# Kernel tuning notes

Measured on AMD Instinct MI355X. Metric: run time of the kernel, lower is better.

The kernel has to match this reference:

```python
import jax, jax.numpy as jnp
import numpy as np

N_X = 32640   # total xlmr subword tokens (64 seqs x 510 tokens)
N_S = 16320   # total stanza word tokens (2 subwords per word)
E = 65280     # dependency edges (bidirectional, avg degree ~4)
D = 768
GCN_DIM = 256
GCN_NUM = 2
POS_DIM = 4
N_UPOS = 17
N_LABEL = 5


def setup_inputs() -> dict:
    key = jax.random.key(0)
    ks = jax.random.split(key, 8)
    x = jax.random.normal(ks[0], (N_X, D), dtype=jnp.float32)
    # mapStanza2Xlmr as segment ids: xlmr token j belongs to stanza word j//2
    seg = jnp.arange(N_X, dtype=jnp.int32) // 2
    edge_index = jax.random.randint(ks[1], (2, E), 0, N_S, dtype=jnp.int32)
    upos_ids = jax.random.randint(ks[2], (N_S,), 0, N_UPOS, dtype=jnp.int32)
    Wc = jax.random.normal(ks[3], (D, GCN_DIM), dtype=jnp.float32) * 0.02
    bc = jnp.zeros((GCN_DIM,), dtype=jnp.float32)
    gcn_W = jax.random.normal(ks[4], (GCN_NUM, GCN_DIM, GCN_DIM), dtype=jnp.float32) * 0.05
    gcn_b = jnp.zeros((GCN_NUM, GCN_DIM), dtype=jnp.float32)
    upos_table = jax.random.normal(ks[5], (N_UPOS, POS_DIM), dtype=jnp.float32)
    Wcls = jax.random.normal(ks[6], (D + GCN_DIM + POS_DIM, N_LABEL), dtype=jnp.float32) * 0.02
    bcls = jnp.zeros((N_LABEL,), dtype=jnp.float32)
    return {"x": x, "seg": seg, "edge_index": edge_index, "upos_ids": upos_ids,
            "Wc": Wc, "bc": bc, "gcn_W": gcn_W, "gcn_b": gcn_b,
            "upos_table": upos_table, "Wcls": Wcls, "bcls": bcls}


def _gcn_conv(h, srcs, dsts, W, b, n):
    # PyG GCNConv: h' = D^-1/2 (A+I) D^-1/2 (h W) + b  (self loops already in srcs/dsts)
    h = h @ W
    deg = jax.ops.segment_sum(jnp.ones_like(dsts, h.dtype), dsts, num_segments=n)
    dinv = jax.lax.rsqrt(deg)  # deg >= 1 because of self loops
    coef = dinv[srcs] * dinv[dsts]
    out = jax.ops.segment_sum(h[srcs] * coef[:, None], dsts, num_segments=n)
    return out + b


def reference(x, seg, edge_index, upos_ids, Wc, bc, gcn_W, gcn_b, upos_table, Wcls, bcls):
    # mapStanza2Xlmr: mean-pool subword embeddings into stanza word embeddings
    cnt = jax.ops.segment_sum(jnp.ones((N_X,), x.dtype), seg, num_segments=N_S)
    stanza = jax.ops.segment_sum(x, seg, num_segments=N_S) / cnt[:, None]  # [N_S, D]
    # GCN over dependency edges (gcn_mode=0: biedges)
    h = stanza @ Wc + bc
    self_idx = jnp.arange(N_S, dtype=edge_index.dtype)
    srcs = jnp.concatenate([edge_index[0], self_idx])
    dsts = jnp.concatenate([edge_index[1], self_idx])
    for i in range(GCN_NUM):
        h = jax.nn.relu(_gcn_conv(h, srcs, dsts, gcn_W[i], gcn_b[i], N_S))
    # POS embedding + concat + relu
    pos = upos_table[upos_ids]                                  # [N_S, POS_DIM]
    info = jax.nn.relu(jnp.concatenate([h, pos], axis=1))       # [N_S, GCN_DIM+POS_DIM]
    # mapXlmr2Stanza: each subword gathers its (single) word's info
    append = info[seg]                                          # [N_X, GCN_DIM+POS_DIM]
    tok = jnp.concatenate([x, append], axis=1)                  # [N_X, 1028]
    logits = jax.nn.relu(tok) @ Wcls + bcls
    return jax.nn.log_softmax(logits, axis=1)
```

## Files before the change

### kernel.cpp

```cpp
#include <hip/hip_runtime.h>

#define NXT 32640
#define NS  16320
#define NE  65280
#define DD  768
#define GD  256
#define NLAB 5
#define CAP 32

typedef __attribute__((ext_vector_type(8))) short bf16x8;
typedef __attribute__((ext_vector_type(4))) float f32x4;

__device__ inline unsigned short f2b(float f) {
    unsigned int u = __float_as_uint(f);
    unsigned int r = (u + 0x7FFFu + ((u >> 16) & 1u)) >> 16;
    return (unsigned short)r;
}
__device__ inline float b2f(unsigned short h) {
    return __uint_as_float((unsigned int)h << 16);
}

__device__ inline void tile_transpose(const float* __restrict__ src, unsigned short* __restrict__ dst,
                                      int K, int k0, int n0, int tid) {
    __shared__ unsigned short tl[64][65];
#pragma unroll
    for (int i = 0; i < 16; ++i) {
        int idx = tid + i * 256;
        int r = idx >> 6, c = idx & 63;
        tl[r][c] = f2b(src[(size_t)(k0 + r) * GD + n0 + c]);
    }
    __syncthreads();
#pragma unroll
    for (int i = 0; i < 16; ++i) {
        int idx = tid + i * 256;
        int rr = idx >> 6, cc = idx & 63;
        dst[(size_t)(n0 + rr) * K + k0 + cc] = tl[cc][rr];
    }
}

__global__ void k_setup(int* __restrict__ cnt,
                        const float* __restrict__ Wc, unsigned short* __restrict__ WcT,
                        const float* __restrict__ gcn_W, unsigned short* __restrict__ WT,
                        const float* __restrict__ Wcls, float* __restrict__ WclsT,
                        const float* __restrict__ upos_table, const float* __restrict__ bcls,
                        float* __restrict__ posLogit) {
    int b = blockIdx.x, t = threadIdx.x;
    if (b < 64) {
        int i = b * 256 + t;
        if (i < NS) cnt[i] = 0;
    } else if (b < 112) {
        int tile = b - 64;
        tile_transpose(Wc, WcT, DD, (tile >> 2) * 64, (tile & 3) * 64, t);
    } else if (b < 128) {
        int tile = b - 112;
        tile_transpose(gcn_W, WT, GD, (tile >> 2) * 64, (tile & 3) * 64, t);
    } else if (b < 144) {
        int tile = b - 128;
        tile_transpose(gcn_W + (size_t)GD * GD, WT + (size_t)GD * GD, GD,
                       (tile >> 2) * 64, (tile & 3) * 64, t);
    } else if (b < 159) {
        int idx = (b - 144) * 256 + t;
        int l = idx / DD, k = idx - l * DD;
        WclsT[idx] = Wcls[(size_t)k * NLAB + l];
    } else {
        if (t < 17 * NLAB) {
            int u = t / NLAB, l = t - u * NLAB;
            float a = bcls[l];
#pragma unroll
            for (int p = 0; p < 4; ++p) {
                float pv = upos_table[u * 4 + p];
                pv = pv > 0.f ? pv : 0.f;
                a += pv * Wcls[(size_t)(DD + GD + p) * NLAB + l];
            }
            posLogit[t] = a;
        }
    }
}

__global__ void k_fill(const int* __restrict__ ei, int* __restrict__ cnt,
                       int* __restrict__ csr_src) {
    int e = blockIdx.x * 256 + threadIdx.x;
    if (e < NE) {
        int dst = ei[NE + e];
        int slot = atomicAdd(&cnt[dst], 1);
        if (slot < CAP) csr_src[(size_t)dst * CAP + slot] = ei[e];
    }
}

__global__ __launch_bounds__(256) void k_xpass(const float* __restrict__ x,
                                               const float* __restrict__ WclsT,
                                               float* __restrict__ partial,
                                               unsigned short* __restrict__ stanza) {
    int w    = blockIdx.x * 4 + (threadIdx.x >> 6);
    int lane = threadIdx.x & 63;
    const float* xr0 = x + (size_t)(2 * w) * DD + lane * 4;
    const float* xr1 = xr0 + DD;
    f32x4 a[3], b[3];
#pragma unroll
    for (int p = 0; p < 3; ++p) {
        a[p] = *(const f32x4*)(xr0 + p * 256);
        b[p] = *(const f32x4*)(xr1 + p * 256);
    }
#pragma unroll
    for (int p = 0; p < 3; ++p) {
        ushort4 o;
        o.x = f2b((a[p][0] + b[p][0]) * 0.5f);
        o.y = f2b((a[p][1] + b[p][1]) * 0.5f);
        o.z = f2b((a[p][2] + b[p][2]) * 0.5f);
        o.w = f2b((a[p][3] + b[p][3]) * 0.5f);
        *(ushort4*)(stanza + (size_t)w * DD + p * 256 + lane * 4) = o;
    }
    f32x4 ra[3], rb[3];
#pragma unroll
    for (int p = 0; p < 3; ++p)
#pragma unroll
        for (int i = 0; i < 4; ++i) {
            ra[p][i] = a[p][i] > 0.f ? a[p][i] : 0.f;
            rb[p][i] = b[p][i] > 0.f ? b[p][i] : 0.f;
        }
    float acc0[NLAB] = {}, acc1[NLAB] = {};
#pragma unroll
    for (int l = 0; l < NLAB; ++l)
#pragma unroll
        for (int p = 0; p < 3; ++p) {
            f32x4 wv = *(const f32x4*)(WclsT + (size_t)l * DD + p * 256 + lane * 4);
#pragma unroll
            for (int i = 0; i < 4; ++i) {
                acc0[l] += ra[p][i] * wv[i];
                acc1[l] += rb[p][i] * wv[i];
            }
        }
#pragma unroll
    for (int off = 32; off > 0; off >>= 1)
#pragma unroll
        for (int l = 0; l < NLAB; ++l) {
            acc0[l] += __shfl_xor(acc0[l], off);
            acc1[l] += __shfl_xor(acc1[l], off);
        }
    if (lane == 0) {
        float* pp = partial + (size_t)w * 2 * NLAB;
#pragma unroll
        for (int l = 0; l < NLAB; ++l) { pp[l] = acc0[l]; pp[NLAB + l] = acc1[l]; }
    }
}

__global__ __launch_bounds__(256) void k_gemm(const unsigned short* __restrict__ A,
                                              const unsigned short* __restrict__ BT,
                                              const float* __restrict__ bias,
                                              unsigned short* __restrict__ out,
                                              int K, int nbn) {
    __shared__ unsigned short lds[1536 * 8];
    const int tid  = threadIdx.x;
    const int lane = tid & 63;
    const int wv   = tid >> 6;
    const int wr   = wv >> 1, wc = wv & 1;
    const int bm   = (blockIdx.x / nbn) * 64;
    const int bn   = (blockIdx.x % nbn) * 128;

    const int g  = tid >> 6, w_ = tid & 63, kc = w_ >> 4, rl = w_ & 15;
    const unsigned short* srcA  = A  + (size_t)(bm + g * 16 + rl) * K + kc * 8;
    const unsigned short* srcB0 = BT + (size_t)(bn      + g * 16 + rl) * K + kc * 8;
    const unsigned short* srcB1 = BT + (size_t)(bn + 64 + g * 16 + rl) * K + kc * 8;

    unsigned short* dA0 = lds + (size_t)tid * 8;
    unsigned short* dA1 = dA0 + 256 * 8;
    unsigned short* dB  = lds + (size_t)(512 + tid) * 8;

    const bf16x8* fA = (const bf16x8*)lds + (wr * 2) * 64 + lane;
    const bf16x8* fB = (const bf16x8*)lds + 512 + wc * 256 + lane;

    f32x4 acc[2][4] = {};
    for (int k0 = 0; k0 < K; k0 += 64) {
        __builtin_amdgcn_global_load_lds(srcA  + k0,      dA0,            16, 0, 0);
        __builtin_amdgcn_global_load_lds(srcA  + k0 + 32, dA1,            16, 0, 0);
        __builtin_amdgcn_global_load_lds(srcB0 + k0,      dB,             16, 0, 0);
        __builtin_amdgcn_global_load_lds(srcB1 + k0,      dB + 256 * 8,   16, 0, 0);
        __builtin_amdgcn_global_load_lds(srcB0 + k0 + 32, dB + 512 * 8,   16, 0, 0);
        __builtin_amdgcn_global_load_lds(srcB1 + k0 + 32, dB + 768 * 8,   16, 0, 0);
        __syncthreads();
#pragma unroll
        for (int kh = 0; kh < 2; ++kh) {
            bf16x8 a0 = fA[kh * 256], a1 = fA[kh * 256 + 64];
            const bf16x8* fb = fB + kh * 512;
            bf16x8 b0 = fb[0], b1 = fb[64], b2 = fb[128], b3 = fb[192];
            acc[0][0] = __builtin_amdgcn_mfma_f32_16x16x32_bf16(a0, b0, acc[0][0], 0, 0, 0);
            acc[0][1] = __builtin_amdgcn_mfma_f32_16x16x32_bf16(a0, b1, acc[0][1], 0, 0, 0);
            acc[0][2] = __builtin_amdgcn_mfma_f32_16x16x32_bf16(a0, b2, acc[0][2], 0, 0, 0);
            acc[0][3] = __builtin_amdgcn_mfma_f32_16x16x32_bf16(a0, b3, acc[0][3], 0, 0, 0);
            acc[1][0] = __builtin_amdgcn_mfma_f32_16x16x32_bf16(a1, b0, acc[1][0], 0, 0, 0);
            acc[1][1] = __builtin_amdgcn_mfma_f32_16x16x32_bf16(a1, b1, acc[1][1], 0, 0, 0);
            acc[1][2] = __builtin_amdgcn_mfma_f32_16x16x32_bf16(a1, b2, acc[1][2], 0, 0, 0);
            acc[1][3] = __builtin_amdgcn_mfma_f32_16x16x32_bf16(a1, b3, acc[1][3], 0, 0, 0);
        }
        __syncthreads();
    }

    const int rl2 = lane & 15, rq = lane >> 4;
#pragma unroll
    for (int m = 0; m < 2; ++m) {
        int row0 = bm + wr * 32 + m * 16 + rq * 4;
#pragma unroll
        for (int n = 0; n < 4; ++n) {
            int col = bn + wc * 64 + n * 16 + rl2;
            float bv = bias ? bias[col] : 0.f;
#pragma unroll
            for (int r = 0; r < 4; ++r)
                out[(size_t)(row0 + r) * GD + col] = f2b(acc[m][n][r] + bv);
        }
    }
}

__global__ void k_gather(const int* __restrict__ cnt, const int* __restrict__ csr_src,
                         const unsigned short* __restrict__ hW,
                         const float* __restrict__ b, unsigned short* __restrict__ hout) {
    int w    = blockIdx.x * 4 + (threadIdx.x >> 6);
    int lane = threadIdx.x & 63;
    int c = cnt[w];
    float dw = rsqrtf((float)c + 1.0f);
    const int* sl = csr_src + (size_t)w * CAP;
    float ax = 0.f, ay = 0.f, az = 0.f, aw = 0.f;
    for (int j = 0; j < c; ++j) {
        int src = sl[j];
        float cf = rsqrtf((float)cnt[src] + 1.0f) * dw;
        ushort4 v = *(const ushort4*)&hW[(size_t)src * GD + lane * 4];
        ax += cf * b2f(v.x); ay += cf * b2f(v.y); az += cf * b2f(v.z); aw += cf * b2f(v.w);
    }
    ushort4 sv = *(const ushort4*)&hW[(size_t)w * GD + lane * 4];
    f32x4 bv = *(const f32x4*)&b[lane * 4];
    float c2 = dw * dw;
    float rx = ax + b2f(sv.x) * c2 + bv[0];
    float ry = ay + b2f(sv.y) * c2 + bv[1];
    float rz = az + b2f(sv.z) * c2 + bv[2];
    float rw = aw + b2f(sv.w) * c2 + bv[3];
    ushort4 o;
    o.x = f2b(rx > 0.f ? rx : 0.f);
    o.y = f2b(ry > 0.f ? ry : 0.f);
    o.z = f2b(rz > 0.f ? rz : 0.f);
    o.w = f2b(rw > 0.f ? rw : 0.f);
    *(ushort4*)&hout[(size_t)w * GD + lane * 4] = o;
}

__global__ void k_gather_final(const int* __restrict__ cnt, const int* __restrict__ csr_src,
                               const unsigned short* __restrict__ hW,
                               const float* __restrict__ b,
                               const float* __restrict__ partial,
                               const int* __restrict__ upos_ids,
                               const float* __restrict__ posLogit,
                               const float* __restrict__ Wcls,
                               float* __restrict__ out) {
    int w    = blockIdx.x * 4 + (threadIdx.x >> 6);
    int lane = threadIdx.x & 63;
    int c = cnt[w];
    float dw = rsqrtf((float)c + 1.0f);
    const int* sl = csr_src + (size_t)w * CAP;
    float ax = 0.f, ay = 0.f, az = 0.f, aw = 0.f;
    for (int j = 0; j < c; ++j) {
        int src = sl[j];
        float cf = rsqrtf((float)cnt[src] + 1.0f) * dw;
        ushort4 v = *(const ushort4*)&hW[(size_t)src * GD + lane * 4];
        ax += cf * b2f(v.x); ay += cf * b2f(v.y); az += cf * b2f(v.z); aw += cf * b2f(v.w);
    }
    ushort4 sv = *(const ushort4*)&hW[(size_t)w * GD + lane * 4];
    f32x4 bv = *(const f32x4*)&b[lane * 4];
    float c2 = dw * dw;
    float hv[4];
    hv[0] = ax + b2f(sv.x) * c2 + bv[0];
    hv[1] = ay + b2f(sv.y) * c2 + bv[1];
    hv[2] = az + b2f(sv.z) * c2 + bv[2];
    hv[3] = aw + b2f(sv.w) * c2 + bv[3];
    float acc[NLAB] = {};
#pragma unroll
    for (int i = 0; i < 4; ++i) {
        float v = hv[i] > 0.f ? hv[i] : 0.f;
        const float* wr = Wcls + (size_t)(DD + lane * 4 + i) * NLAB;
#pragma unroll
        for (int l = 0; l < NLAB; ++l) acc[l] += v * wr[l];
    }
#pragma unroll
    for (int off = 32; off > 0; off >>= 1)
#pragma unroll
        for (int l = 0; l < NLAB; ++l) acc[l] += __shfl_xor(acc[l], off);
    if (lane == 0) {
        const float* pl = posLogit + (size_t)upos_ids[w] * NLAB;
        const float* pp = partial + (size_t)w * 2 * NLAB;
#pragma unroll
        for (int t = 0; t < 2; ++t) {
            float lg[NLAB];
#pragma unroll
            for (int l = 0; l < NLAB; ++l) lg[l] = acc[l] + pp[t * NLAB + l] + pl[l];
            float m = lg[0];
#pragma unroll
            for (int l = 1; l < NLAB; ++l) m = fmaxf(m, lg[l]);
            float s = 0.f;
#pragma unroll
            for (int l = 0; l < NLAB; ++l) s += __expf(lg[l] - m);
            float lse = __logf(s) + m;
            float* op = out + (size_t)(2 * w + t) * NLAB;
#pragma unroll
            for (int l = 0; l < NLAB; ++l) op[l] = lg[l] - lse;
        }
    }
}

extern "C" void kernel_launch(void* const* d_in, const int* in_sizes, int n_in,
                              void* d_out, int out_size, void* d_ws, size_t ws_size,
                              hipStream_t stream) {
    const float* x          = (const float*)d_in[0];
    const int*   ei         = (const int*)d_in[2];
    const int*   upos_ids   = (const int*)d_in[3];
    const float* Wc         = (const float*)d_in[4];
    const float* bc         = (const float*)d_in[5];
    const float* gcn_W      = (const float*)d_in[6];
    const float* gcn_b      = (const float*)d_in[7];
    const float* upos_table = (const float*)d_in[8];
    const float* Wcls       = (const float*)d_in[9];
    const float* bcls       = (const float*)d_in[10];
    float* out = (float*)d_out;

    char* ws = (char*)d_ws;
    float* partial          = (float*)ws;            ws += (size_t)NXT * NLAB * 4;
    float* WclsT            = (float*)ws;            ws += (size_t)NLAB * DD * 4;
    float* posLogit         = (float*)ws;            ws += (size_t)17 * NLAB * 4;
    unsigned short* stanza  = (unsigned short*)ws;   ws += (size_t)NS * DD * 2;
    unsigned short* h_bf    = (unsigned short*)ws;   ws += (size_t)NS * GD * 2;
    unsigned short* hW_bf   = (unsigned short*)ws;   ws += (size_t)NS * GD * 2;
    unsigned short* WcT     = (unsigned short*)ws;   ws += (size_t)DD * GD * 2;
    unsigned short* WT      = (unsigned short*)ws;   ws += (size_t)2 * GD * GD * 2;
    int* cnt                = (int*)ws;              ws += (size_t)NS * 4;
    int* csr_src            = (int*)ws;              ws += (size_t)NS * CAP * 4;

    k_setup<<<160, 256, 0, stream>>>(cnt, Wc, WcT, gcn_W, WT, Wcls, WclsT,
                                     upos_table, bcls, posLogit);
    k_fill<<<(NE + 255) / 256, 256, 0, stream>>>(ei, cnt, csr_src);
    k_xpass<<<NS / 4, 256, 0, stream>>>(x, WclsT, partial, stanza);
    k_gemm<<<(NS / 64) * 2, 256, 0, stream>>>(stanza, WcT, bc, h_bf, DD, 2);
    k_gemm<<<(NS / 64) * 2, 256, 0, stream>>>(h_bf, WT, nullptr, hW_bf, GD, 2);
    k_gather<<<NS / 4, 256, 0, stream>>>(cnt, csr_src, hW_bf, gcn_b, h_bf);
    k_gemm<<<(NS / 64) * 2, 256, 0, stream>>>(h_bf, WT + (size_t)GD * GD, nullptr, hW_bf, GD, 2);
    k_gather_final<<<NS / 4, 256, 0, stream>>>(cnt, csr_src, hW_bf, gcn_b + GD,
                                               partial, upos_ids, posLogit, Wcls, out);
}
```

Baseline: 117.1 us.

## Fuse mean-pooling, Wc GEMM, classifier partial logits and CSR fill into one kernel

Merges the x-pass (mean pooling plus per-token classifier dot products), the first dense GEMM and the edge CSR fill into a single launch. Pooled bf16 rows go straight into LDS as the A operand, so the bf16 stanza intermediate is never written to or read back from global memory. The per-token classifier logits now run on MFMA against a zero-padded bf16 Wcls layout built in setup. The cost is more LDS per block, a bf16 rounding of the relu'd x before the classifier dot product, and a single 64-row tile computing all 256 output columns per block.

```diff
diff --git a/kernel.cpp b/kernel.cpp
--- a/kernel.cpp
+++ b/kernel.cpp
@@ -9,6 +9,7 @@
 #define CAP 32
 
 typedef __attribute__((ext_vector_type(8))) short bf16x8;
+typedef __attribute__((ext_vector_type(8))) unsigned short u16x8;
 typedef __attribute__((ext_vector_type(4))) float f32x4;
 
 __device__ inline unsigned short f2b(float f) {
@@ -41,7 +42,7 @@
 __global__ void k_setup(int* __restrict__ cnt,
                         const float* __restrict__ Wc, unsigned short* __restrict__ WcT,
                         const float* __restrict__ gcn_W, unsigned short* __restrict__ WT,
-                        const float* __restrict__ Wcls, float* __restrict__ WclsT,
+                        const float* __restrict__ Wcls, unsigned short* __restrict__ WclsF,
                         const float* __restrict__ upos_table, const float* __restrict__ bcls,
                         float* __restrict__ posLogit) {
     int b = blockIdx.x, t = threadIdx.x;
@@ -58,10 +59,12 @@
         int tile = b - 128;
         tile_transpose(gcn_W + (size_t)GD * GD, WT + (size_t)GD * GD, GD,
                        (tile >> 2) * 64, (tile & 3) * 64, t);
-    } else if (b < 159) {
+    } else if (b < 192) {
         int idx = (b - 144) * 256 + t;
-        int l = idx / DD, k = idx - l * DD;
-        WclsT[idx] = Wcls[(size_t)k * NLAB + l];
+        int i = idx & 7, l = (idx >> 3) & 63, s = idx >> 9;
+        int col = l & 15;
+        int k = s * 32 + (l >> 4) * 8 + i;
+        WclsF[idx] = (col < NLAB) ? f2b(Wcls[(size_t)k * NLAB + col]) : 0;
     } else {
         if (t < 17 * NLAB) {
             int u = t / NLAB, l = t - u * NLAB;
@@ -77,70 +80,113 @@
     }
 }
 
-__global__ void k_fill(const int* __restrict__ ei, int* __restrict__ cnt,
-                       int* __restrict__ csr_src) {
-    int e = blockIdx.x * 256 + threadIdx.x;
-    if (e < NE) {
-        int dst = ei[NE + e];
-        int slot = atomicAdd(&cnt[dst], 1);
-        if (slot < CAP) csr_src[(size_t)dst * CAP + slot] = ei[e];
-    }
-}
-
-__global__ __launch_bounds__(256) void k_xpass(const float* __restrict__ x,
-                                               const float* __restrict__ WclsT,
-                                               float* __restrict__ partial,
-                                               unsigned short* __restrict__ stanza) {
-    int w    = blockIdx.x * 4 + (threadIdx.x >> 6);
-    int lane = threadIdx.x & 63;
-    const float* xr0 = x + (size_t)(2 * w) * DD + lane * 4;
+__global__ __launch_bounds__(256) void k_mega0(const float* __restrict__ x,
+                                               const unsigned short* __restrict__ WcT,
+                                               const unsigned short* __restrict__ WclsF,
+                                               const float* __restrict__ bc,
+                                               const int* __restrict__ ei,
+                                               int* __restrict__ cnt, int* __restrict__ csr_src,
+                                               unsigned short* __restrict__ h_bf,
+                                               float* __restrict__ partial) {
+    __shared__ unsigned short lds[3584 * 8];
+    const int tid = threadIdx.x;
+    if (blockIdx.x >= 255) {
+        int e = (blockIdx.x - 255) * 256 + tid;
+        if (e < NE) {
+            int dst = ei[NE + e];
+            int slot = atomicAdd(&cnt[dst], 1);
+            if (slot < CAP) csr_src[(size_t)dst * CAP + slot] = ei[e];
+        }
+        return;
+    }
+    const int lane = tid & 63;
+    const int wv   = tid >> 6;
+    const int wr   = wv >> 1, wc = wv & 1;
+    const int bm   = blockIdx.x * 64;
+
+    const int g = tid >> 6, kc = (tid >> 4) & 3, rl = tid & 15;
+    const int w_loc = g * 16 + rl;
+    const float* xr0 = x + (size_t)(2 * (bm + w_loc)) * DD + kc * 8;
     const float* xr1 = xr0 + DD;
-    f32x4 a[3], b[3];
-#pragma unroll
-    for (int p = 0; p < 3; ++p) {
-        a[p] = *(const f32x4*)(xr0 + p * 256);
-        b[p] = *(const f32x4*)(xr1 + p * 256);
-    }
-#pragma unroll
-    for (int p = 0; p < 3; ++p) {
-        ushort4 o;
-        o.x = f2b((a[p][0] + b[p][0]) * 0.5f);
-        o.y = f2b((a[p][1] + b[p][1]) * 0.5f);
-        o.z = f2b((a[p][2] + b[p][2]) * 0.5f);
-        o.w = f2b((a[p][3] + b[p][3]) * 0.5f);
-        *(ushort4*)(stanza + (size_t)w * DD + p * 256 + lane * 4) = o;
-    }
-    f32x4 ra[3], rb[3];
-#pragma unroll
-    for (int p = 0; p < 3; ++p)
-#pragma unroll
-        for (int i = 0; i < 4; ++i) {
-            ra[p][i] = a[p][i] > 0.f ? a[p][i] : 0.f;
-            rb[p][i] = b[p][i] > 0.f ? b[p][i] : 0.f;
-        }
-    float acc0[NLAB] = {}, acc1[NLAB] = {};
-#pragma unroll
-    for (int l = 0; l < NLAB; ++l)
-#pragma unroll
-        for (int p = 0; p < 3; ++p) {
-            f32x4 wv = *(const f32x4*)(WclsT + (size_t)l * DD + p * 256 + lane * 4);
+    const int t0 = 2 * w_loc, t1 = t0 + 1;
+    const int ap0 = (t0 >> 4) * 64 + kc * 16 + (t0 & 15);
+    const int ap1 = (t1 >> 4) * 64 + kc * 16 + (t1 & 15);
+    const unsigned short* srcB = WcT + (size_t)(g * 16 + rl) * DD + kc * 8;
+
+    const bf16x8* ldsv = (const bf16x8*)lds;
+    f32x4 acc[2][8] = {};
+    f32x4 acc_lg[2] = {};
+
+    for (int it = 0; it < 12; ++it) {
+        const int k0 = it * 64;
+#pragma unroll
+        for (int nh = 0; nh < 4; ++nh)
+#pragma unroll
+            for (int kh = 0; kh < 2; ++kh)
+                __builtin_amdgcn_global_load_lds(srcB + (size_t)nh * 64 * DD + k0 + kh * 32,
+                                                 lds + (size_t)(1536 + (nh * 2 + kh) * 256 + tid) * 8,
+                                                 16, 0, 0);
+#pragma unroll
+        for (int kh = 0; kh < 2; ++kh) {
+            f32x4 v0a = *(const f32x4*)(xr0 + k0 + kh * 32);
+            f32x4 v0b = *(const f32x4*)(xr0 + k0 + kh * 32 + 4);
+            f32x4 v1a = *(const f32x4*)(xr1 + k0 + kh * 32);
+            f32x4 v1b = *(const f32x4*)(xr1 + k0 + kh * 32 + 4);
+            u16x8 pool, ra, rb;
 #pragma unroll
             for (int i = 0; i < 4; ++i) {
-                acc0[l] += ra[p][i] * wv[i];
-                acc1[l] += rb[p][i] * wv[i];
+                pool[i]     = f2b((v0a[i] + v1a[i]) * 0.5f);
+                pool[4 + i] = f2b((v0b[i] + v1b[i]) * 0.5f);
+                ra[i]     = f2b(v0a[i] > 0.f ? v0a[i] : 0.f);
+                ra[4 + i] = f2b(v0b[i] > 0.f ? v0b[i] : 0.f);
+                rb[i]     = f2b(v1a[i] > 0.f ? v1a[i] : 0.f);
+                rb[4 + i] = f2b(v1b[i] > 0.f ? v1b[i] : 0.f);
             }
-        }
-#pragma unroll
-    for (int off = 32; off > 0; off >>= 1)
-#pragma unroll
-        for (int l = 0; l < NLAB; ++l) {
-            acc0[l] += __shfl_xor(acc0[l], off);
-            acc1[l] += __shfl_xor(acc1[l], off);
-        }
-    if (lane == 0) {
-        float* pp = partial + (size_t)w * 2 * NLAB;
-#pragma unroll
-        for (int l = 0; l < NLAB; ++l) { pp[l] = acc0[l]; pp[NLAB + l] = acc1[l]; }
+            *(u16x8*)(lds + (size_t)(kh * 256 + tid) * 8) = pool;
+            *(u16x8*)(lds + (size_t)(512 + kh * 512 + ap0) * 8) = ra;
+            *(u16x8*)(lds + (size_t)(512 + kh * 512 + ap1) * 8) = rb;
+        }
+        __syncthreads();
+#pragma unroll
+        for (int kh = 0; kh < 2; ++kh) {
+            bf16x8 a0 = ldsv[kh * 256 + (wr * 2 + 0) * 64 + lane];
+            bf16x8 a1 = ldsv[kh * 256 + (wr * 2 + 1) * 64 + lane];
+            bf16x8 at0 = ldsv[512 + kh * 512 + (wv * 2 + 0) * 64 + lane];
+            bf16x8 at1 = ldsv[512 + kh * 512 + (wv * 2 + 1) * 64 + lane];
+            bf16x8 bl = *(const bf16x8*)(WclsF + (size_t)(it * 2 + kh) * 512 + lane * 8);
+            acc_lg[0] = __builtin_amdgcn_mfma_f32_16x16x32_bf16(at0, bl, acc_lg[0], 0, 0, 0);
+            acc_lg[1] = __builtin_amdgcn_mfma_f32_16x16x32_bf16(at1, bl, acc_lg[1], 0, 0, 0);
+#pragma unroll
+            for (int n = 0; n < 8; ++n) {
+                bf16x8 b = ldsv[1536 + ((wc * 2 + (n >> 2)) * 2 + kh) * 256 + (n & 3) * 64 + lane];
+                acc[0][n] = __builtin_amdgcn_mfma_f32_16x16x32_bf16(a0, b, acc[0][n], 0, 0, 0);
+                acc[1][n] = __builtin_amdgcn_mfma_f32_16x16x32_bf16(a1, b, acc[1][n], 0, 0, 0);
+            }
+        }
+        __syncthreads();
+    }
+
+    const int rl2 = lane & 15, rq = lane >> 4;
+#pragma unroll
+    for (int m = 0; m < 2; ++m) {
+        int row0 = bm + wr * 32 + m * 16 + rq * 4;
+#pragma unroll
+        for (int n = 0; n < 8; ++n) {
+            int col = wc * 128 + n * 16 + rl2;
+            float bv = bc[col];
+#pragma unroll
+            for (int r = 0; r < 4; ++r)
+                h_bf[(size_t)(row0 + r) * GD + col] = f2b(acc[m][n][r] + bv);
+        }
+    }
+    if (rl2 < NLAB) {
+#pragma unroll
+        for (int tf = 0; tf < 2; ++tf) {
+            int tok0 = 2 * bm + wv * 32 + tf * 16 + rq * 4;
+#pragma unroll
+            for (int r = 0; r < 4; ++r)
+                partial[(size_t)(tok0 + r) * NLAB + rl2] = acc_lg[tf][r];
+        }
     }
 }
 
@@ -319,21 +365,18 @@
 
     char* ws = (char*)d_ws;
     float* partial          = (float*)ws;            ws += (size_t)NXT * NLAB * 4;
-    float* WclsT            = (float*)ws;            ws += (size_t)NLAB * DD * 4;
     float* posLogit         = (float*)ws;            ws += (size_t)17 * NLAB * 4;
-    unsigned short* stanza  = (unsigned short*)ws;   ws += (size_t)NS * DD * 2;
     unsigned short* h_bf    = (unsigned short*)ws;   ws += (size_t)NS * GD * 2;
     unsigned short* hW_bf   = (unsigned short*)ws;   ws += (size_t)NS * GD * 2;
     unsigned short* WcT     = (unsigned short*)ws;   ws += (size_t)DD * GD * 2;
     unsigned short* WT      = (unsigned short*)ws;   ws += (size_t)2 * GD * GD * 2;
+    unsigned short* WclsF   = (unsigned short*)ws;   ws += (size_t)24 * 512 * 2;
     int* cnt                = (int*)ws;              ws += (size_t)NS * 4;
     int* csr_src            = (int*)ws;              ws += (size_t)NS * CAP * 4;
 
-    k_setup<<<160, 256, 0, stream>>>(cnt, Wc, WcT, gcn_W, WT, Wcls, WclsT,
+    k_setup<<<193, 256, 0, stream>>>(cnt, Wc, WcT, gcn_W, WT, Wcls, WclsF,
                                      upos_table, bcls, posLogit);
-    k_fill<<<(NE + 255) / 256, 256, 0, stream>>>(ei, cnt, csr_src);
-    k_xpass<<<NS / 4, 256, 0, stream>>>(x, WclsT, partial, stanza);
-    k_gemm<<<(NS / 64) * 2, 256, 0, stream>>>(stanza, WcT, bc, h_bf, DD, 2);
+    k_mega0<<<510, 256, 0, stream>>>(x, WcT, WclsF, bc, ei, cnt, csr_src, h_bf, partial);
     k_gemm<<<(NS / 64) * 2, 256, 0, stream>>>(h_bf, WT, nullptr, hW_bf, GD, 2);
     k_gather<<<NS / 4, 256, 0, stream>>>(cnt, csr_src, hW_bf, gcn_b, h_bf);
     k_gemm<<<(NS / 64) * 2, 256, 0, stream>>>(h_bf, WT + (size_t)GD * GD, nullptr, hW_bf, GD, 2);
```

Result: no change. 115.0 us (-1.9%).
